# Optimization experiments

Measured on AMD Instinct MI355X. Metric: run time of the kernel, lower is better.

## Reference

```python
import jax, jax.numpy as jnp
import numpy as np

D_MODEL, H, KD, VD = 1024, 16, 64, 64
B, N, M_LEN = 4, 2048, 2048


def setup_inputs() -> dict:
    key = jax.random.key(0)
    ks = jax.random.split(key, 6)
    X = jax.random.normal(ks[0], (B, N, D_MODEL), dtype=jnp.float32)
    M = jax.random.normal(ks[1], (B, M_LEN, D_MODEL), dtype=jnp.float32)
    mask = jnp.zeros((B, 1, N, M_LEN), dtype=jnp.float32)
    P_q = jax.random.normal(ks[2], (H, D_MODEL, KD), dtype=jnp.float32)
    P_k = jax.random.normal(ks[3], (D_MODEL, KD), dtype=jnp.float32)
    P_v = jax.random.normal(ks[4], (D_MODEL, VD), dtype=jnp.float32)
    P_o = jax.random.normal(ks[5], (H, D_MODEL, VD), dtype=jnp.float32)
    return {"X": X, "M": M, "mask": mask, "P_q": P_q, "P_k": P_k, "P_v": P_v, "P_o": P_o}


def reference(X, M, mask, P_q, P_k, P_v, P_o):
    # Per-head query projection; shared K/V projections (MQA)
    Q = jnp.einsum('bnd,hdk->bhnk', X, P_q)
    K = jnp.einsum('bmd,dk->bmk', M, P_k)
    V = jnp.einsum('bmd,dv->bmv', M, P_v)
    logits = jnp.einsum('bhnk,bmk->bhnm', Q, K) + mask
    weights = jax.nn.softmax(logits, axis=-1)
    O = jnp.einsum('bhnm,bmv->bhnv', weights, V)
    Y = jnp.einsum('bhnv,hdv->bnd', O, P_o)
    return Y
```

## Files before the change

kernel.cpp:

```cpp
#include <hip/hip_runtime.h>
#include <cstdint>
#include <cstddef>

typedef unsigned short u16;
typedef unsigned int   u32;
typedef short s16x8 __attribute__((ext_vector_type(8)));
typedef float f32x4 __attribute__((ext_vector_type(4)));

#define B_   4
#define H_   16
#define N_   2048
#define M_   2048
#define D_   1024
#define ROWS 8192

__device__ __forceinline__ u16 f2bf(float x){
  u32 u = __builtin_bit_cast(u32, x);
  u = (u + 0x7fffu + ((u >> 16) & 1u)) >> 16;
  return (u16)u;
}
__device__ __forceinline__ float bf2f(u16 h){
  u32 u = ((u32)h) << 16;
  return __builtin_bit_cast(float, u);
}
__device__ __forceinline__ void split2(float v, u16 &h, u16 &l){
  h = f2bf(v);
  l = f2bf(v - bf2f(h));
}
__device__ __forceinline__ void gload16(const void* g, void* l){
  __builtin_amdgcn_global_load_lds((const __attribute__((address_space(1))) u32*)g,
                                   (__attribute__((address_space(3))) u32*)l, 16, 0, 0);
}
__device__ __forceinline__ f32x4 mfma16(s16x8 a, s16x8 b, f32x4 c){
  return __builtin_amdgcn_mfma_f32_16x16x32_bf16(a, b, c, 0, 0, 0);
}

__global__ void split_xm(const float* __restrict__ X, const float* __restrict__ Mi,
                         u16* __restrict__ Xh, u16* __restrict__ Xl,
                         u16* __restrict__ Mh, u16* __restrict__ Ml){
  const int n4 = ROWS * D_ / 4;
  for (int i = blockIdx.x * blockDim.x + threadIdx.x; i < n4; i += gridDim.x * blockDim.x){
    float4 x = ((const float4*)X)[i];
    float4 m = ((const float4*)Mi)[i];
    ushort4 xh, xl, mh, ml;
    split2(x.x, xh.x, xl.x); split2(x.y, xh.y, xl.y);
    split2(x.z, xh.z, xl.z); split2(x.w, xh.w, xl.w);
    split2(m.x, mh.x, ml.x); split2(m.y, mh.y, ml.y);
    split2(m.z, mh.z, ml.z); split2(m.w, mh.w, ml.w);
    ((ushort4*)Xh)[i] = xh; ((ushort4*)Xl)[i] = xl;
    ((ushort4*)Mh)[i] = mh; ((ushort4*)Ml)[i] = ml;
  }
}

__global__ void transform_w(const float* __restrict__ Pq, const float* __restrict__ Pk,
                            const float* __restrict__ Pv, const float* __restrict__ Po,
                            u16* __restrict__ PqTh, u16* __restrict__ PqTl,
                            u16* __restrict__ PkvTh, u16* __restrict__ PkvTl,
                            u16* __restrict__ WoTh, u16* __restrict__ WoTl){
  const int TOT = 1048576 + 131072 + 1048576;
  for (int gid = blockIdx.x * blockDim.x + threadIdx.x; gid < TOT; gid += gridDim.x * blockDim.x){
    float v; u16 *oh, *ol; int oidx;
    if (gid < 1048576){
      int c = gid >> 10, d = gid & 1023;
      v = Pq[(size_t)(c >> 6) * 65536 + d * 64 + (c & 63)];
      oh = PqTh; ol = PqTl; oidx = gid;
    } else if (gid < 1048576 + 131072){
      int t = gid - 1048576; int c = t >> 10, d = t & 1023;
      v = (c < 64) ? Pk[d * 64 + c] : Pv[d * 64 + (c - 64)];
      oh = PkvTh; ol = PkvTl; oidx = t;
    } else {
      int t = gid - (1048576 + 131072); int dd = t >> 10, hv = t & 1023;
      v = Po[(size_t)(hv >> 6) * 65536 + dd * 64 + (hv & 63)];
      oh = WoTh; ol = WoTl; oidx = t;
    }
    u16 h, l; split2(v, h, l);
    oh[oidx] = h; ol[oidx] = l;
  }
}

template<int MODE>
__global__ __launch_bounds__(256, 2)
void gemm3(const u16* __restrict__ Ah, const u16* __restrict__ Al,
           const u16* __restrict__ Bh, const u16* __restrict__ Bl,
           void* __restrict__ o0, void* __restrict__ o1, void* __restrict__ o2){
  __shared__ __align__(16) u16 lds[2][4][128 * 32];
  const int tid = threadIdx.x;
  const int lane = tid & 63;
  const int w = tid >> 6;
  const int wr = w >> 1, wc = w & 1;
  const int br0 = blockIdx.y * 128;
  const int bc0 = blockIdx.x * 128;

  const u16* srcs[4] = {Ah, Al, Bh, Bl};

  auto stage = [&](int buf, int s){
    const int k0 = s * 32;
#pragma unroll
    for (int t = 0; t < 4; t++){
      const u16* src = srcs[t];
      const int rbase = (t >= 2) ? bc0 : br0;
#pragma unroll
      for (int it = 0; it < 2; it++){
        const int c1k = w * 2 + it;
        const int ci = c1k * 64 + lane;
        const int row = ci >> 2;
        const int gs = (ci & 3) ^ ((row >> 1) & 3);
        gload16(src + (size_t)(rbase + row) * 1024 + k0 + gs * 8,
                &lds[buf][t][c1k * 512]);
      }
    }
  };

  f32x4 acc[4][4];
#pragma unroll
  for (int i = 0; i < 4; i++)
#pragma unroll
    for (int j = 0; j < 4; j++) acc[i][j] = f32x4{0.f, 0.f, 0.f, 0.f};

  stage(0, 0);
  for (int s = 0; s < 32; s++){
    __syncthreads();
    if (s + 1 < 32) stage((s + 1) & 1, s + 1);
    const int buf = s & 1;
    const int g = lane >> 4;
    s16x8 fah[4], fal[4], fbh[4], fbl[4];
#pragma unroll
    for (int i = 0; i < 4; i++){
      const int ra = wr * 64 + i * 16 + (lane & 15);
      const int oa = ra * 64 + ((g ^ ((ra >> 1) & 3)) * 16);
      fah[i] = *(const s16x8*)((const char*)&lds[buf][0][0] + oa);
      fal[i] = *(const s16x8*)((const char*)&lds[buf][1][0] + oa);
      const int rb = wc * 64 + i * 16 + (lane & 15);
      const int ob = rb * 64 + ((g ^ ((rb >> 1) & 3)) * 16);
      fbh[i] = *(const s16x8*)((const char*)&lds[buf][2][0] + ob);
      fbl[i] = *(const s16x8*)((const char*)&lds[buf][3][0] + ob);
    }
#pragma unroll
    for (int i = 0; i < 4; i++)
#pragma unroll
      for (int j = 0; j < 4; j++){
        acc[i][j] = mfma16(fah[i], fbh[j], acc[i][j]);
        acc[i][j] = mfma16(fah[i], fbl[j], acc[i][j]);
        acc[i][j] = mfma16(fal[i], fbh[j], acc[i][j]);
      }
  }

#pragma unroll
  for (int i = 0; i < 4; i++){
#pragma unroll
    for (int j = 0; j < 4; j++){
#pragma unroll
      for (int r = 0; r < 4; r++){
        const int row = br0 + wr * 64 + i * 16 + (lane >> 4) * 4 + r;
        const int col = bc0 + wc * 64 + j * 16 + (lane & 15);
        const float v = acc[i][j][r];
        if (MODE == 0){
          const int b = row >> 11, n = row & 2047;
          const int h = col >> 6,  k = col & 63;
          const size_t idx = ((size_t)(b * H_ + h) * N_ + n) * 64 + k;
          u16 hh, ll; split2(v, hh, ll);
          ((u16*)o0)[idx] = hh; ((u16*)o1)[idx] = ll;
        } else if (MODE == 1){
          if (col < 64){
            const size_t idx = (size_t)row * 64 + col;
            u16 hh, ll; split2(v, hh, ll);
            ((u16*)o0)[idx] = hh; ((u16*)o1)[idx] = ll;
          } else {
            const int b = row >> 11, m = row & 2047;
            const size_t idx = (size_t)b * (64 * 2048) + (size_t)(col - 64) * 2048 + m;
            ((u16*)o2)[idx] = f2bf(v);
          }
        } else {
          ((float*)o0)[(size_t)row * 1024 + col] = v;
        }
      }
    }
  }
}

__global__ __launch_bounds__(256, 3)
void attn(const u16* __restrict__ Qh, const u16* __restrict__ Ql,
          const u16* __restrict__ Kh, const u16* __restrict__ Kl,
          const u16* __restrict__ VT, const float* __restrict__ mask,
          u16* __restrict__ Oh, u16* __restrict__ Ol){
  __shared__ __align__(16) u16  khb[2][2048];
  __shared__ __align__(16) u16  klb[2][2048];
  __shared__ __align__(16) u16  vb [2][2048];
  __shared__ __align__(16) float mb[2][1024];
  __shared__ __align__(16) u16  pbuf[4][1280];

  const int t = threadIdx.x;
  const int lane = t & 63;
  const int w = t >> 6;
  const int g = lane >> 4;
  const int c = lane & 15;
  const int r8 = blockIdx.x & 7;
  const int i8 = blockIdx.x >> 3;
  const int wgid = r8 * 128 + i8;
  const int b   = wgid >> 8;
  const int rem = wgid & 255;
  const int q5  = rem >> 2;
  const int hg  = rem & 3;
  const int h   = hg * 4 + w;
  const int q0  = q5 * 32;

  const u16* qbh = Qh + ((size_t)(b * H_ + h) * N_) * 64;
  const u16* qbl = Ql + ((size_t)(b * H_ + h) * N_) * 64;
  const u16* kgh = Kh + (size_t)b * M_ * 64;
  const u16* kgl = Kl + (size_t)b * M_ * 64;
  const u16* vg  = VT + (size_t)b * 64 * M_;
  const float* mg = mask + (size_t)b * N_ * M_;

  const int sr = t >> 3, sj = t & 7;
  const int vr = t >> 2, vj = t & 3;
  const size_t koff = (size_t)sr * 64 + (size_t)((sj ^ (sr & 7)) * 8);
  const size_t moff = (size_t)(q0 + sr) * M_ + (size_t)((sj ^ (sr & 7)) * 4);
  const size_t voff = (size_t)vr * M_ + (size_t)((vj ^ (vr & 3)) * 8);

  auto stage = [&](int buf, int m0){
    gload16(kgh + (size_t)m0 * 64 + koff, &khb[buf][t * 8]);
    gload16(kgl + (size_t)m0 * 64 + koff, &klb[buf][t * 8]);
    gload16(vg + m0 + voff,               &vb[buf][t * 8]);
    gload16(mg + m0 + moff,               &mb[buf][t * 4]);
  };

  s16x8 fqh[2][2], fql[2][2];
#pragma unroll
  for (int qt = 0; qt < 2; qt++)
#pragma unroll
    for (int kc = 0; kc < 2; kc++){
      const size_t off = (size_t)(q0 + qt * 16 + c) * 64 + kc * 32 + g * 8;
      fqh[qt][kc] = *(const s16x8*)(qbh + off);
      fql[qt][kc] = *(const s16x8*)(qbl + off);
    }

  f32x4 acc[2][4];
#pragma unroll
  for (int qt = 0; qt < 2; qt++)
#pragma unroll
    for (int vt = 0; vt < 4; vt++) acc[qt][vt] = f32x4{0.f, 0.f, 0.f, 0.f};
  float mrun[2] = {-INFINITY, -INFINITY};
  float lrun[2] = {0.f, 0.f};
  u16* pl = &pbuf[w][0];

  stage(0, 0);
  for (int it = 0; it < 64; ++it){
    const int m0 = it * 32;
    const int cur = it & 1;
    __syncthreads();
    if (it < 63) stage(cur ^ 1, m0 + 32);

    const char* kh_ = (const char*)khb[cur];
    const char* kl_ = (const char*)klb[cur];
    s16x8 kfh[2][2], kfl[2][2];
#pragma unroll
    for (int mt = 0; mt < 2; mt++)
#pragma unroll
      for (int kc = 0; kc < 2; kc++){
        const int p = (mt * 16 + c) * 128 + (((kc * 4 + g) ^ (c & 7)) * 16);
        kfh[mt][kc] = *(const s16x8*)(kh_ + p);
        kfl[mt][kc] = *(const s16x8*)(kl_ + p);
      }
    const char* v_ = (const char*)vb[cur];
    s16x8 fv[4];
#pragma unroll
    for (int vt = 0; vt < 4; vt++)
      fv[vt] = *(const s16x8*)(v_ + (vt * 16 + c) * 64 + ((g ^ (c & 3)) * 16));

    f32x4 S[2][2];
#pragma unroll
    for (int qt = 0; qt < 2; qt++)
#pragma unroll
      for (int mt = 0; mt < 2; mt++){
        f32x4 a = f32x4{0.f, 0.f, 0.f, 0.f};
        a = mfma16(kfh[mt][0], fqh[qt][0], a);
        a = mfma16(kfh[mt][1], fqh[qt][1], a);
        a = mfma16(kfl[mt][0], fqh[qt][0], a);
        a = mfma16(kfl[mt][1], fqh[qt][1], a);
        a = mfma16(kfh[mt][0], fql[qt][0], a);
        a = mfma16(kfh[mt][1], fql[qt][1], a);
        S[qt][mt] = a;
      }
    const char* m_ = (const char*)mb[cur];
#pragma unroll
    for (int qt = 0; qt < 2; qt++)
#pragma unroll
      for (int mt = 0; mt < 2; mt++){
        const f32x4 mk = *(const f32x4*)(m_ + (qt * 16 + c) * 128 + (((mt * 4 + g) ^ (c & 7)) * 16));
        S[qt][mt] = S[qt][mt] + mk;
      }

#pragma unroll
    for (int qt = 0; qt < 2; qt++){
      float rmax = fmaxf(fmaxf(fmaxf(S[qt][0][0], S[qt][0][1]), fmaxf(S[qt][0][2], S[qt][0][3])),
                         fmaxf(fmaxf(S[qt][1][0], S[qt][1][1]), fmaxf(S[qt][1][2], S[qt][1][3])));
      rmax = fmaxf(rmax, __shfl_xor(rmax, 16, 64));
      rmax = fmaxf(rmax, __shfl_xor(rmax, 32, 64));
      const float mnew = fmaxf(mrun[qt], rmax);
      const float sc = __expf(mrun[qt] - mnew);
      mrun[qt] = mnew;
#pragma unroll
      for (int vt = 0; vt < 4; vt++){
        acc[qt][vt][0] *= sc; acc[qt][vt][1] *= sc;
        acc[qt][vt][2] *= sc; acc[qt][vt][3] *= sc;
      }
      float psum = 0.f;
#pragma unroll
      for (int mt = 0; mt < 2; mt++){
        float p0 = __expf(S[qt][mt][0] - mnew);
        float p1 = __expf(S[qt][mt][1] - mnew);
        float p2 = __expf(S[qt][mt][2] - mnew);
        float p3 = __expf(S[qt][mt][3] - mnew);
        psum += (p0 + p1) + (p2 + p3);
        ushort4 pk;
        pk.x = f2bf(p0); pk.y = f2bf(p1); pk.z = f2bf(p2); pk.w = f2bf(p3);
        *(ushort4*)((char*)pl + (qt * 16 + c) * 80 + mt * 32 + g * 8) = pk;
      }
      lrun[qt] = lrun[qt] * sc + psum;
    }
    s16x8 pb0 = *(const s16x8*)((const char*)pl + c * 80 + g * 16);
    s16x8 pb1 = *(const s16x8*)((const char*)pl + (16 + c) * 80 + g * 16);
#pragma unroll
    for (int vt = 0; vt < 4; vt++){
      acc[0][vt] = mfma16(fv[vt], pb0, acc[0][vt]);
      acc[1][vt] = mfma16(fv[vt], pb1, acc[1][vt]);
    }
  }

#pragma unroll
  for (int qt = 0; qt < 2; qt++){
    float tot = lrun[qt];
    tot += __shfl_xor(tot, 16, 64);
    tot += __shfl_xor(tot, 32, 64);
    const float inv = 1.0f / tot;
    const int qq = q0 + qt * 16 + c;
    const size_t rowbase = ((size_t)(b * N_ + qq)) * 1024 + h * 64;
#pragma unroll
    for (int vt = 0; vt < 4; vt++){
      ushort4 ph, plo;
      u16 hh, ll;
      split2(acc[qt][vt][0] * inv, hh, ll); ph.x = hh; plo.x = ll;
      split2(acc[qt][vt][1] * inv, hh, ll); ph.y = hh; plo.y = ll;
      split2(acc[qt][vt][2] * inv, hh, ll); ph.z = hh; plo.z = ll;
      split2(acc[qt][vt][3] * inv, hh, ll); ph.w = hh; plo.w = ll;
      const size_t idx = rowbase + vt * 16 + g * 4;
      *(ushort4*)(Oh + idx) = ph;
      *(ushort4*)(Ol + idx) = plo;
    }
  }
}

extern "C" void kernel_launch(void* const* d_in, const int* in_sizes, int n_in,
                              void* d_out, int out_size, void* d_ws, size_t ws_size,
                              hipStream_t stream){
  const float* X  = (const float*)d_in[0];
  const float* Mi = (const float*)d_in[1];
  const float* mask = (const float*)d_in[2];
  const float* Pq = (const float*)d_in[3];
  const float* Pk = (const float*)d_in[4];
  const float* Pv = (const float*)d_in[5];
  const float* Po = (const float*)d_in[6];
  float* Y = (float*)d_out;

  char* ws = (char*)d_ws;
  auto alloc = [&](size_t bytes) -> char* {
    char* p = ws;
    ws += (bytes + 255) & ~(size_t)255;
    return p;
  };
  const size_t SZ_XM = (size_t)ROWS * D_ * 2;
  u16* Xh = (u16*)alloc(SZ_XM);
  u16* Xl = (u16*)alloc(SZ_XM);
  u16* Mh = (u16*)alloc(SZ_XM);
  u16* Ml = (u16*)alloc(SZ_XM);
  u16* PqTh = (u16*)alloc(1024 * 1024 * 2);
  u16* PqTl = (u16*)alloc(1024 * 1024 * 2);
  u16* PkvTh = (u16*)alloc(128 * 1024 * 2);
  u16* PkvTl = (u16*)alloc(128 * 1024 * 2);
  u16* WoTh = (u16*)alloc(1024 * 1024 * 2);
  u16* WoTl = (u16*)alloc(1024 * 1024 * 2);
  u16* Qh = (u16*)alloc(SZ_XM);
  u16* Ql = (u16*)alloc(SZ_XM);
  u16* Kh = (u16*)alloc((size_t)B_ * M_ * 64 * 2);
  u16* Kl = (u16*)alloc((size_t)B_ * M_ * 64 * 2);
  u16* VT = (u16*)alloc((size_t)B_ * M_ * 64 * 2);
  u16* Oh = (u16*)alloc(SZ_XM);
  u16* Ol = (u16*)alloc(SZ_XM);
  if ((size_t)(ws - (char*)d_ws) > ws_size) return;

  split_xm<<<2048, 256, 0, stream>>>(X, Mi, Xh, Xl, Mh, Ml);
  transform_w<<<1024, 256, 0, stream>>>(Pq, Pk, Pv, Po, PqTh, PqTl, PkvTh, PkvTl, WoTh, WoTl);
  gemm3<1><<<dim3(1, 64), 256, 0, stream>>>(Mh, Ml, PkvTh, PkvTl, Kh, Kl, VT);
  gemm3<0><<<dim3(8, 64), 256, 0, stream>>>(Xh, Xl, PqTh, PqTl, Qh, Ql, nullptr);
  attn<<<1024, 256, 0, stream>>>(Qh, Ql, Kh, Kl, VT, mask, Oh, Ol);
  gemm3<2><<<dim3(8, 64), 256, 0, stream>>>(Oh, Ol, WoTh, WoTl, Y, nullptr, nullptr);
}
```

Measured before the change: 550.8 us.

## Keep softmax probabilities in registers via permuted K rows; skip unchanged rescales

Reorders the K tile rows during staging so that each lane's S accumulator values line up with the B-operand layout of the PV MFMA. The bf16 probabilities can then be packed straight into registers instead of passing through a per-wave LDS buffer, and the mask read index is adjusted to match. Also skips the accumulator rescale when no lane's running max grows, uses the hardware bf16 conversion, and raises the occupancy hint to 4 waves per SIMD. This removes LDS round-trips and conversion ALU work, at the risk of register spills from the tighter launch bound.

```diff
diff --git a/kernel.cpp b/kernel.cpp
--- a/kernel.cpp
+++ b/kernel.cpp
@@ -1,4 +1,5 @@
 #include <hip/hip_runtime.h>
+#include <hip/hip_bf16.h>
 #include <cstdint>
 #include <cstddef>
 
@@ -26,6 +27,9 @@
 __device__ __forceinline__ void split2(float v, u16 &h, u16 &l){
   h = f2bf(v);
   l = f2bf(v - bf2f(h));
+}
+__device__ __forceinline__ u16 fbhw(float x){
+  return __builtin_bit_cast(u16, __float2bfloat16(x));
 }
 __device__ __forceinline__ void gload16(const void* g, void* l){
   __builtin_amdgcn_global_load_lds((const __attribute__((address_space(1))) u32*)g,
@@ -178,7 +182,7 @@
   }
 }
 
-__global__ __launch_bounds__(256, 3)
+__global__ __launch_bounds__(256, 4)
 void attn(const u16* __restrict__ Qh, const u16* __restrict__ Ql,
           const u16* __restrict__ Kh, const u16* __restrict__ Kl,
           const u16* __restrict__ VT, const float* __restrict__ mask,
@@ -187,7 +191,6 @@
   __shared__ __align__(16) u16  klb[2][2048];
   __shared__ __align__(16) u16  vb [2][2048];
   __shared__ __align__(16) float mb[2][1024];
-  __shared__ __align__(16) u16  pbuf[4][1280];
 
   const int t = threadIdx.x;
   const int lane = t & 63;
@@ -213,7 +216,8 @@
 
   const int sr = t >> 3, sj = t & 7;
   const int vr = t >> 2, vj = t & 3;
-  const size_t koff = (size_t)sr * 64 + (size_t)((sj ^ (sr & 7)) * 8);
+  const int prow = ((sr >> 2) & 3) * 8 + ((sr >> 4) & 1) * 4 + (sr & 3);
+  const size_t koff = (size_t)prow * 64 + (size_t)((sj ^ (sr & 7)) * 8);
   const size_t moff = (size_t)(q0 + sr) * M_ + (size_t)((sj ^ (sr & 7)) * 4);
   const size_t voff = (size_t)vr * M_ + (size_t)((vj ^ (vr & 3)) * 8);
 
@@ -241,7 +245,6 @@
     for (int vt = 0; vt < 4; vt++) acc[qt][vt] = f32x4{0.f, 0.f, 0.f, 0.f};
   float mrun[2] = {-INFINITY, -INFINITY};
   float lrun[2] = {0.f, 0.f};
-  u16* pl = &pbuf[w][0];
 
   stage(0, 0);
   for (int it = 0; it < 64; ++it){
@@ -286,7 +289,7 @@
     for (int qt = 0; qt < 2; qt++)
 #pragma unroll
       for (int mt = 0; mt < 2; mt++){
-        const f32x4 mk = *(const f32x4*)(m_ + (qt * 16 + c) * 128 + (((mt * 4 + g) ^ (c & 7)) * 16));
+        const f32x4 mk = *(const f32x4*)(m_ + (qt * 16 + c) * 128 + (((2 * g + mt) ^ (c & 7)) * 16));
         S[qt][mt] = S[qt][mt] + mk;
       }
 
@@ -296,34 +299,34 @@
                          fmaxf(fmaxf(S[qt][1][0], S[qt][1][1]), fmaxf(S[qt][1][2], S[qt][1][3])));
       rmax = fmaxf(rmax, __shfl_xor(rmax, 16, 64));
       rmax = fmaxf(rmax, __shfl_xor(rmax, 32, 64));
-      const float mnew = fmaxf(mrun[qt], rmax);
-      const float sc = __expf(mrun[qt] - mnew);
-      mrun[qt] = mnew;
-#pragma unroll
-      for (int vt = 0; vt < 4; vt++){
-        acc[qt][vt][0] *= sc; acc[qt][vt][1] *= sc;
-        acc[qt][vt][2] *= sc; acc[qt][vt][3] *= sc;
+      if (__any(rmax > mrun[qt])){
+        const float mnew = fmaxf(mrun[qt], rmax);
+        const float sc = __expf(mrun[qt] - mnew);
+        mrun[qt] = mnew;
+        lrun[qt] *= sc;
+#pragma unroll
+        for (int vt = 0; vt < 4; vt++){
+          acc[qt][vt][0] *= sc; acc[qt][vt][1] *= sc;
+          acc[qt][vt][2] *= sc; acc[qt][vt][3] *= sc;
+        }
       }
       float psum = 0.f;
+      u16 pk[8];
 #pragma unroll
       for (int mt = 0; mt < 2; mt++){
-        float p0 = __expf(S[qt][mt][0] - mnew);
-        float p1 = __expf(S[qt][mt][1] - mnew);
-        float p2 = __expf(S[qt][mt][2] - mnew);
-        float p3 = __expf(S[qt][mt][3] - mnew);
+        float p0 = __expf(S[qt][mt][0] - mrun[qt]);
+        float p1 = __expf(S[qt][mt][1] - mrun[qt]);
+        float p2 = __expf(S[qt][mt][2] - mrun[qt]);
+        float p3 = __expf(S[qt][mt][3] - mrun[qt]);
         psum += (p0 + p1) + (p2 + p3);
-        ushort4 pk;
-        pk.x = f2bf(p0); pk.y = f2bf(p1); pk.z = f2bf(p2); pk.w = f2bf(p3);
-        *(ushort4*)((char*)pl + (qt * 16 + c) * 80 + mt * 32 + g * 8) = pk;
-      }
-      lrun[qt] = lrun[qt] * sc + psum;
-    }
-    s16x8 pb0 = *(const s16x8*)((const char*)pl + c * 80 + g * 16);
-    s16x8 pb1 = *(const s16x8*)((const char*)pl + (16 + c) * 80 + g * 16);
-#pragma unroll
-    for (int vt = 0; vt < 4; vt++){
-      acc[0][vt] = mfma16(fv[vt], pb0, acc[0][vt]);
-      acc[1][vt] = mfma16(fv[vt], pb1, acc[1][vt]);
+        pk[mt * 4 + 0] = fbhw(p0); pk[mt * 4 + 1] = fbhw(p1);
+        pk[mt * 4 + 2] = fbhw(p2); pk[mt * 4 + 3] = fbhw(p3);
+      }
+      lrun[qt] += psum;
+      const s16x8 pb = __builtin_bit_cast(s16x8, pk);
+#pragma unroll
+      for (int vt = 0; vt < 4; vt++)
+        acc[qt][vt] = mfma16(fv[vt], pb, acc[qt][vt]);
     }
   }
 
```

Measured after the change: 494.7 us. 10.2% less time.
